# Optimization experiments

Measured on AMD Instinct MI355X. Metric: run time of the kernel, lower is better.

The kernel has to match this reference:

```python
import jax, jax.numpy as jnp
import numpy as np

EPS = 1e-5

def _bn(x, g, b, axes):
    m = jnp.mean(x, axes, keepdims=True)
    v = jnp.var(x, axes, keepdims=True)
    return (x - m) * jax.lax.rsqrt(v + EPS) * g + b

def _fps(p, m):
    # farthest point sampling: p [B,N,3] -> int32 indices [B,m]
    B, N, _ = p.shape
    def step(carry, _):
        mind, last = carry
        lastp = jnp.take_along_axis(p, last[:, None, None], axis=1)[:, 0]  # [B,3]
        d = jnp.sum((p - lastp[:, None, :]) ** 2, axis=-1)                 # [B,N]
        mind = jnp.minimum(mind, d)
        nxt = jnp.argmax(mind, axis=1).astype(jnp.int32)
        return (mind, nxt), last
    init = (jnp.full((B, N), jnp.inf, p.dtype), jnp.zeros((B,), jnp.int32))
    _, idxs = jax.lax.scan(step, init, None, length=m)  # [m,B]
    return idxs.T

def _gather(x, idx):
    # x [B,N,C], idx [B,...] -> [B,...,C]
    B, C = x.shape[0], x.shape[-1]
    flat = idx.reshape(B, -1)
    out = jnp.take_along_axis(x, flat[:, :, None], axis=1)
    return out.reshape(idx.shape + (C,))

def _transition_down(p, h, W, g, b, stride, nsample):
    # p [B,N,3], h [B,N,C] -> new_p [B,N//stride,3], y [B,N//stride,Cout]
    B, N, _ = p.shape
    M = N // stride
    idx = _fps(p, M)
    new_p = _gather(p, idx)                                               # [B,M,3]
    d = jnp.sum((new_p[:, :, None, :] - p[:, None, :, :]) ** 2, axis=-1)  # [B,M,N]
    _, nidx = jax.lax.top_k(-d, nsample)                                  # [B,M,k]
    gp = _gather(p, nidx) - new_p[:, :, None, :]                          # rel xyz [B,M,k,3]
    gx = _gather(h, nidx)                                                 # [B,M,k,C]
    feat = jnp.concatenate([gp, gx], axis=-1)                             # with_xyz=True
    y = jnp.einsum('bmkc,cd->bmkd', feat, W)
    y = jax.nn.relu(_bn(y, g, b, (0, 1, 2)))
    return new_p, jnp.max(y, axis=2)                                      # MaxPool1d(nsample)

def _forward(x, W1, g1, b1, W2, g2, b2, W3, g3, b3, W4, g4, b4, W5, g5, b5,
             Wc1, bc1, gc1, hc1, Wc2, bc2, gc2, hc2, Wc3, bc3):
    p = x[..., :3]                                    # in_channels == 3 -> features = xyz
    h = jnp.einsum('bnc,cd->bnd', p, W1)
    h = jax.nn.relu(_bn(h, g1, b1, (0, 1)))           # enc1: stride=1
    p, h = _transition_down(p, h, W2, g2, b2, 4, 16)  # enc2
    p, h = _transition_down(p, h, W3, g3, b3, 4, 16)  # enc3
    p, h = _transition_down(p, h, W4, g4, b4, 4, 16)  # enc4
    p, h = _transition_down(p, h, W5, g5, b5, 4, 16)  # enc5
    z = jnp.mean(h, axis=1)                           # segment-mean pool -> [B,512]
    z = jax.nn.relu(_bn(z @ Wc1 + bc1, gc1, hc1, (0,)))   # Dropout = identity (eval)
    z = jax.nn.relu(_bn(z @ Wc2 + bc2, gc2, hc2, (0,)))
    return z @ Wc3 + bc3                              # [B,40]

def setup_inputs() -> dict:
    key = jax.random.key(0)
    ks = jax.random.split(key, 16)
    B, N = 16, 4096
    def lin(k, fi, fo):
        return (jax.random.normal(k, (fi, fo), jnp.float32) / np.sqrt(fi)).astype(jnp.float32)
    inp = {"x": jax.random.normal(ks[0], (B, N, 3), jnp.float32)}
    planes = [32, 64, 128, 256, 512]
    ins = [3, 3 + 32, 3 + 64, 3 + 128, 3 + 256]
    for i, (fi, fo) in enumerate(zip(ins, planes), start=1):
        inp[f"W{i}"] = lin(ks[i], fi, fo)
        inp[f"g{i}"] = jnp.ones((fo,), jnp.float32)
        inp[f"b{i}"] = jnp.zeros((fo,), jnp.float32)
    dims = [(512, 256), (256, 128), (128, 40)]
    for j, (fi, fo) in enumerate(dims, start=1):
        inp[f"Wc{j}"] = lin(ks[5 + j], fi, fo)
        inp[f"bc{j}"] = jnp.zeros((fo,), jnp.float32)
        if j < 3:
            inp[f"gc{j}"] = jnp.ones((fo,), jnp.float32)
            inp[f"hc{j}"] = jnp.zeros((fo,), jnp.float32)
    return inp

def reference(x, W1, g1, b1, W2, g2, b2, W3, g3, b3, W4, g4, b4, W5, g5, b5,
              Wc1, bc1, gc1, hc1, Wc2, bc2, gc2, hc2, Wc3, bc3):
    return _forward(x, W1, g1, b1, W2, g2, b2, W3, g3, b3, W4, g4, b4, W5, g5, b5,
                    Wc1, bc1, gc1, hc1, Wc2, bc2, gc2, hc2, Wc3, bc3)
```

## Files before the change

### kernel.cpp

```cpp
#include <hip/hip_runtime.h>
#include <math.h>
#include <float.h>

#define BN_EPS 1e-5f

__device__ __forceinline__ float sqdist_exact(float dx, float dy, float dz) {
  return __fadd_rn(__fadd_rn(__fmul_rn(dx, dx), __fmul_rn(dy, dy)), __fmul_rn(dz, dz));
}

#define DPP_STEP(CTRL)                                                                   \
  {                                                                                      \
    unsigned int nhi = (unsigned int)__builtin_amdgcn_update_dpp((int)khi, (int)khi,     \
                                                                 CTRL, 0xf, 0xf, false); \
    unsigned int nlo = (unsigned int)__builtin_amdgcn_update_dpp((int)klo, (int)klo,     \
                                                                 CTRL, 0xf, 0xf, false); \
    unsigned long long nk = (((unsigned long long)nhi) << 32) | nlo;                     \
    if (nk > wk) { wk = nk; khi = nhi; klo = nlo; }                                      \
  }

template <int P, int NW>
__device__ __forceinline__ void fps_body(const float* __restrict__ pb,
                                         float* __restrict__ newp_b,
                                         float* spts, float* snew,
                                         unsigned long long* slots, int t) {
  constexpr int BS = NW * 64;
  constexpr int N = P * BS;
  constexpr int M = N / 4;
  const int wv = t >> 6;
  const int lane = t & 63;
  float px[P], py[P], pz[P], md[P];
#pragma unroll
  for (int j = 0; j < P; j++) {
    int i = j * BS + t;
    float x = pb[3 * i], y = pb[3 * i + 1], z = pb[3 * i + 2];
    px[j] = x; py[j] = y; pz[j] = z; md[j] = INFINITY;
    spts[3 * i] = x; spts[3 * i + 1] = y; spts[3 * i + 2] = z;
  }
  float lx = pb[0], ly = pb[1], lz = pb[2];
  if (t == 0) {
    if constexpr (NW > 1) {
      snew[0] = lx; snew[1] = ly; snew[2] = lz;
    } else {
      newp_b[0] = lx; newp_b[1] = ly; newp_b[2] = lz;
    }
  }

  for (int r = 1; r < M; r++) {
    float bv; int bi;
    {
      float d0 = sqdist_exact(px[0] - lx, py[0] - ly, pz[0] - lz);
      float m0 = fminf(md[0], d0);
      md[0] = m0;
      bv = m0; bi = t;
    }
#pragma unroll
    for (int j = 1; j < P; j++) {
      float d = sqdist_exact(px[j] - lx, py[j] - ly, pz[j] - lz);
      float m = fminf(md[j], d);
      md[j] = m;
      if (m > bv) { bv = m; bi = j * BS + t; }
    }
    unsigned int khi = __float_as_uint(bv);
    unsigned int klo = ~(unsigned int)bi;
    unsigned long long wk = (((unsigned long long)khi) << 32) | klo;
    DPP_STEP(0x111);
    DPP_STEP(0x112);
    DPP_STEP(0x114);
    DPP_STEP(0x118);
    DPP_STEP(0x142);
    DPP_STEP(0x143);
    unsigned int gidx;
    if constexpr (NW == 1) {
      unsigned int wlo = (unsigned int)__builtin_amdgcn_readlane((int)wk, 63);
      gidx = ~wlo;
    } else {
      unsigned long long* base = slots + (r & 1) * NW;
      if (lane == 63) base[wv] = wk;
      __syncthreads();
      unsigned long long fk = base[0];
#pragma unroll
      for (int w = 1; w < NW; w++) {
        unsigned long long k2 = base[w];
        if (k2 > fk) fk = k2;
      }
      gidx = ~(unsigned int)fk;
    }
    lx = spts[3 * gidx];
    ly = spts[3 * gidx + 1];
    lz = spts[3 * gidx + 2];
    if (t == 0) {
      if constexpr (NW > 1) {
        snew[3 * r] = lx; snew[3 * r + 1] = ly; snew[3 * r + 2] = lz;
      } else {
        newp_b[3 * r] = lx; newp_b[3 * r + 1] = ly; newp_b[3 * r + 2] = lz;
      }
    }
  }
  if constexpr (NW > 1) {
    __syncthreads();
    for (int i = t; i < M * 3; i += BS) newp_b[i] = snew[i];
  }
}

__device__ __forceinline__ void knn_body(const float* __restrict__ p,
                                         const float* __restrict__ newp,
                                         int N, int M, int BM,
                                         int* __restrict__ nidx,
                                         int gwid, int lane) {
  if (gwid >= BM) return;
  int b = gwid / M;
  const float* pb = p + (size_t)b * N * 3;
  float qx = newp[(size_t)gwid * 3], qy = newp[(size_t)gwid * 3 + 1], qz = newp[(size_t)gwid * 3 + 2];
  float bd[16];
  int bi[16];
#pragma unroll
  for (int s = 0; s < 16; s++) { bd[s] = INFINITY; bi[s] = 0x7FFFFFFF; }
  for (int c = lane; c < N; c += 64) {
    float d = sqdist_exact(pb[3 * c] - qx, pb[3 * c + 1] - qy, pb[3 * c + 2] - qz);
    if (d < bd[15]) {
      bd[15] = d; bi[15] = c;
#pragma unroll
      for (int s = 15; s >= 1; --s) {
        bool sw = bd[s] < bd[s - 1];
        if (sw) {
          float tf = bd[s]; bd[s] = bd[s - 1]; bd[s - 1] = tf;
          int ti = bi[s]; bi[s] = bi[s - 1]; bi[s - 1] = ti;
        }
      }
    }
  }
  int out = 0;
  for (int r = 0; r < 16; r++) {
    float v = bd[0]; int ii = bi[0];
    float mv = v; int mi = ii;
#pragma unroll
    for (int m = 1; m < 64; m <<= 1) {
      float v2 = __shfl_xor(mv, m);
      int i2 = __shfl_xor(mi, m);
      if (v2 < mv || (v2 == mv && i2 < mi)) { mv = v2; mi = i2; }
    }
    if (mi == ii) {
#pragma unroll
      for (int s = 0; s < 15; s++) { bd[s] = bd[s + 1]; bi[s] = bi[s + 1]; }
      bd[15] = INFINITY; bi[15] = 0x7FFFFFFF;
    }
    if (lane == r) out = mi;
  }
  if (lane < 16) nidx[(size_t)gwid * 16 + lane] = out;
}

__device__ __forceinline__ void stats_body(const float* __restrict__ v, int n, int D,
                                           float* __restrict__ partial, float* sm,
                                           int bid, int nb, int t) {
  int tid = bid * 256 + t;
  int stride = 256 * nb;
  float s = 0.f, q = 0.f;
  for (int i = tid; i < n; i += stride) { float a = v[i]; s += a; q += a * a; }
  int c = tid % D;
  for (int i = t; i < 2 * D; i += 256) sm[i] = 0.f;
  __syncthreads();
  atomicAdd(&sm[c], s);
  atomicAdd(&sm[D + c], q);
  __syncthreads();
  for (int i = t; i < 2 * D; i += 256)
    atomicAdd(&partial[(bid & 63) * 2 * D + i], sm[i]);
}

__device__ __forceinline__ void gemm_body(
    float* sm, const float* __restrict__ p, const float* __restrict__ h,
    const float* __restrict__ newp, const int* __restrict__ nidx,
    const float* __restrict__ W, float* __restrict__ ymax, float* __restrict__ ymin,
    float* __restrict__ partial, int N, int M, int BM, int Ch, int Cpad, int D,
    int Gseq, int bid, int t) {
  int Ctot = Ch + 3;
  int TD = D < 256 ? D : 256;
  int Gpar = 256 / TD;
  float* sfeat = sm;
  float* sstat = sm + Gpar * 16 * Cpad;
  for (int i = t; i < 2 * D; i += 256) sstat[i] = 0.f;
  int mloc = t / TD;
  int dbase = t % TD;
  int DV = D / TD;
  __syncthreads();
  for (int s = 0; s < Gseq; s++) {
    int grp0 = (bid * Gseq + s) * Gpar;
    if (grp0 >= BM) break;
    int nf = Gpar * 16 * Cpad;
    for (int i = t; i < nf; i += 256) {
      int c = i % Cpad;
      int rk = i / Cpad;
      int k = rk & 15;
      int g = rk >> 4;
      int grp = grp0 + g;
      float val = 0.f;
      if (grp < BM && c < Ctot) {
        int b = grp / M;
        int nb = nidx[(size_t)grp * 16 + k];
        if (c < 3)
          val = p[((size_t)b * N + nb) * 3 + c] - newp[(size_t)grp * 3 + c];
        else
          val = h[((size_t)b * N + nb) * Ch + (c - 3)];
      }
      sfeat[i] = val;
    }
    __syncthreads();
    int grp = grp0 + mloc;
    bool act = grp < BM;
    const float* fr = sfeat + mloc * 16 * Cpad;
    for (int dv = 0; dv < DV; ++dv) {
      int d = dbase + (dv << 8);
      float acc[16];
#pragma unroll
      for (int k = 0; k < 16; k++) acc[k] = 0.f;
      for (int c = 0; c < Cpad; c += 4) {
        float w0 = (c < Ctot) ? W[(size_t)c * D + d] : 0.f;
        float w1 = (c + 1 < Ctot) ? W[(size_t)(c + 1) * D + d] : 0.f;
        float w2 = (c + 2 < Ctot) ? W[(size_t)(c + 2) * D + d] : 0.f;
        float w3 = (c + 3 < Ctot) ? W[(size_t)(c + 3) * D + d] : 0.f;
#pragma unroll
        for (int k = 0; k < 16; k++) {
          const float4 f = *reinterpret_cast<const float4*>(fr + k * Cpad + c);
          acc[k] += f.x * w0 + f.y * w1 + f.z * w2 + f.w * w3;
        }
      }
      if (act) {
        float ssum = 0.f, ssq = 0.f, amax = -INFINITY, amin = INFINITY;
#pragma unroll
        for (int k = 0; k < 16; k++) {
          float a = acc[k];
          ssum += a; ssq += a * a;
          amax = fmaxf(amax, a); amin = fminf(amin, a);
        }
        ymax[(size_t)grp * D + d] = amax;
        ymin[(size_t)grp * D + d] = amin;
        atomicAdd(&sstat[d], ssum);
        atomicAdd(&sstat[D + d], ssq);
      }
    }
    __syncthreads();
  }
  for (int i = t; i < 2 * D; i += 256)
    atomicAdd(&partial[(bid & 63) * 2 * D + i], sstat[i]);
}

__global__ void __launch_bounds__(256) fused_fps1_mlp1_kernel(
    const float* __restrict__ x, float* __restrict__ newp,
    const float* __restrict__ W1, float* __restrict__ h1, int rows) {
  __shared__ float spts[4096 * 3];
  __shared__ float snew[1024 * 3];
  __shared__ unsigned long long slots[8];
  const int t = threadIdx.x;
  if (blockIdx.x < 16) {
    fps_body<16, 4>(x + (size_t)blockIdx.x * 4096 * 3, newp + (size_t)blockIdx.x * 1024 * 3,
                    spts, snew, slots, t);
  } else {
    int tid = (blockIdx.x - 16) * 256 + t;
    int row = tid >> 5;
    int d = tid & 31;
    if (row < rows) {
      float x0 = x[row * 3 + 0], x1 = x[row * 3 + 1], x2 = x[row * 3 + 2];
      h1[row * 32 + d] = x0 * W1[d] + x1 * W1[32 + d] + x2 * W1[64 + d];
    }
  }
}

__global__ void __launch_bounds__(256) fused_fks_kernel(
    const float* __restrict__ fp, float* __restrict__ fnewp,
    const float* __restrict__ kp, const float* __restrict__ knewp,
    int kN, int kM, int kBM, int* __restrict__ knidx, int nKnn,
    const float* __restrict__ sv, int sn, int sD, float* __restrict__ spartial, int nStats) {
  __shared__ float spts[1024 * 3];
  __shared__ float snew[256 * 3];
  __shared__ unsigned long long slots[8];
  __shared__ float ssm[64];
  const int t = threadIdx.x;
  const int bid = blockIdx.x;
  if (bid < 16) {
    fps_body<4, 4>(fp + (size_t)bid * 1024 * 3, fnewp + (size_t)bid * 256 * 3,
                   spts, snew, slots, t);
  } else if (bid < 16 + nKnn) {
    int gwid = ((bid - 16) * 256 + t) >> 6;
    knn_body(kp, knewp, kN, kM, kBM, knidx, gwid, t & 63);
  } else {
    stats_body(sv, sn, sD, spartial, ssm, bid - 16 - nKnn, nStats, t);
  }
}

template <int P, int NW>
__global__ void __launch_bounds__(256) fused_gfk_kernel(
    const float* __restrict__ p, const float* __restrict__ h,
    const float* __restrict__ newp, const int* __restrict__ nidx,
    const float* __restrict__ W, float* __restrict__ ymax, float* __restrict__ ymin,
    float* __restrict__ partial, int N, int M, int BM, int Ch, int Cpad, int D,
    int Gseq, int nGemm,
    const float* __restrict__ fp, float* __restrict__ fnewp, int nFps,
    const float* __restrict__ kp, const float* __restrict__ knewp,
    int kN, int kM, int kBM, int* __restrict__ knidx) {
  constexpr int FBS = NW * 64;
  constexpr int FN = P * FBS;
  constexpr int FM = FN / 4;
  __shared__ float spts[FN * 3];
  __shared__ float snew[NW > 1 ? FM * 3 : 1];
  __shared__ unsigned long long slots[NW > 1 ? 2 * NW : 2];
  extern __shared__ float sm[];
  const int t = threadIdx.x;
  const int bid = blockIdx.x;
  if (bid < nGemm) {
    gemm_body(sm, p, h, newp, nidx, W, ymax, ymin, partial,
              N, M, BM, Ch, Cpad, D, Gseq, bid, t);
  } else if (bid < nGemm + nFps) {
    int fb = bid - nGemm;
    if (NW > 1 || t < 64) {
      fps_body<P, NW>(fp + (size_t)fb * FN * 3, fnewp + (size_t)fb * FM * 3,
                      spts, snew, slots, t);
    }
  } else {
    int gwid = ((bid - nGemm - nFps) * 256 + t) >> 6;
    knn_body(kp, knewp, kN, kM, kBM, knidx, gwid, t & 63);
  }
}

__global__ void __launch_bounds__(256) gemm_kernel(
    const float* __restrict__ p, const float* __restrict__ h, const float* __restrict__ newp,
    const int* __restrict__ nidx, const float* __restrict__ W,
    float* __restrict__ ymax, float* __restrict__ ymin, float* __restrict__ partial,
    int N, int M, int BM, int Ch, int Cpad, int D, int Gseq) {
  extern __shared__ float sm[];
  gemm_body(sm, p, h, newp, nidx, W, ymax, ymin, partial,
            N, M, BM, Ch, Cpad, D, Gseq, blockIdx.x, threadIdx.x);
}

__global__ void __launch_bounds__(256) bn_fused_kernel(
    const float* __restrict__ partial, const float* __restrict__ g,
    const float* __restrict__ b, float cnt, int D,
    float* __restrict__ vmax, const float* __restrict__ vmin, int n) {
  extern __shared__ float ss[];
  int t = threadIdx.x;
  for (int d = t; d < D; d += 256) {
    float s = 0.f, q = 0.f;
    for (int j = 0; j < 64; j++) { s += partial[j * 2 * D + d]; q += partial[j * 2 * D + D + d]; }
    float mean = s / cnt;
    float var = fmaxf(q / cnt - mean * mean, 0.f);
    float sc = g[d] * rsqrtf(var + BN_EPS);
    ss[d] = sc;
    ss[D + d] = b[d] - mean * sc;
  }
  __syncthreads();
  int tid = blockIdx.x * 256 + t;
  int stride = 256 * gridDim.x;
  for (int i = tid; i < n; i += stride) {
    int d = i % D;
    float sc = ss[d], sh = ss[D + d];
    float v = (sc >= 0.f) ? vmax[i] : vmin[i];
    vmax[i] = fmaxf(v * sc + sh, 0.f);
  }
}

__global__ void __launch_bounds__(512) classifier_kernel(
    const float* __restrict__ h4,
    const float* __restrict__ Wc1, const float* __restrict__ bc1,
    const float* __restrict__ gc1, const float* __restrict__ hc1,
    const float* __restrict__ Wc2, const float* __restrict__ bc2,
    const float* __restrict__ gc2, const float* __restrict__ hc2,
    const float* __restrict__ Wc3, const float* __restrict__ bc3,
    float* __restrict__ out) {
  __shared__ float z[16 * 512];
  __shared__ float z1[16 * 256];
  __shared__ float z2[16 * 128];
  __shared__ float sc[256], sh[256];
  int t = threadIdx.x;
  for (int i = t; i < 16 * 512; i += 512) {
    int b = i >> 9, c = i & 511;
    float s = 0.f;
    for (int k = 0; k < 16; k++) s += h4[((size_t)b * 16 + k) * 512 + c];
    z[i] = s * (1.f / 16.f);
  }
  __syncthreads();
  for (int i = t; i < 16 * 256; i += 512) {
    int b = i >> 8, d = i & 255;
    float a = bc1[d];
    for (int c = 0; c < 512; c++) a += z[(b << 9) + c] * Wc1[c * 256 + d];
    z1[i] = a;
  }
  __syncthreads();
  if (t < 256) {
    float s = 0.f, q = 0.f;
    for (int b = 0; b < 16; b++) { float a = z1[(b << 8) + t]; s += a; q += a * a; }
    float mean = s * (1.f / 16.f);
    float var = fmaxf(q * (1.f / 16.f) - mean * mean, 0.f);
    float scl = gc1[t] * rsqrtf(var + BN_EPS);
    sc[t] = scl; sh[t] = hc1[t] - mean * scl;
  }
  __syncthreads();
  for (int i = t; i < 16 * 256; i += 512) {
    int d = i & 255;
    z1[i] = fmaxf(z1[i] * sc[d] + sh[d], 0.f);
  }
  __syncthreads();
  for (int i = t; i < 16 * 128; i += 512) {
    int b = i >> 7, d = i & 127;
    float a = bc2[d];
    for (int c = 0; c < 256; c++) a += z1[(b << 8) + c] * Wc2[c * 128 + d];
    z2[i] = a;
  }
  __syncthreads();
  if (t < 128) {
    float s = 0.f, q = 0.f;
    for (int b = 0; b < 16; b++) { float a = z2[(b << 7) + t]; s += a; q += a * a; }
    float mean = s * (1.f / 16.f);
    float var = fmaxf(q * (1.f / 16.f) - mean * mean, 0.f);
    float scl = gc2[t] * rsqrtf(var + BN_EPS);
    sc[t] = scl; sh[t] = hc2[t] - mean * scl;
  }
  __syncthreads();
  for (int i = t; i < 16 * 128; i += 512) {
    int d = i & 127;
    z2[i] = fmaxf(z2[i] * sc[d] + sh[d], 0.f);
  }
  __syncthreads();
  for (int i = t; i < 640; i += 512) {
    int b = i / 40, d = i % 40;
    float a = bc3[d];
    for (int c = 0; c < 128; c++) a += z2[(b << 7) + c] * Wc3[c * 40 + d];
    out[i] = a;
  }
}

extern "C" void kernel_launch(void* const* d_in, const int* in_sizes, int n_in,
                              void* d_out, int out_size, void* d_ws, size_t ws_size,
                              hipStream_t stream) {
  (void)in_sizes; (void)n_in; (void)out_size; (void)ws_size;
  const float* x   = (const float*)d_in[0];
  const float* W1  = (const float*)d_in[1];
  const float* g1  = (const float*)d_in[2];
  const float* b1  = (const float*)d_in[3];
  const float* W2  = (const float*)d_in[4];
  const float* g2  = (const float*)d_in[5];
  const float* b2  = (const float*)d_in[6];
  const float* W3  = (const float*)d_in[7];
  const float* g3  = (const float*)d_in[8];
  const float* b3  = (const float*)d_in[9];
  const float* W4  = (const float*)d_in[10];
  const float* g4  = (const float*)d_in[11];
  const float* b4  = (const float*)d_in[12];
  const float* W5  = (const float*)d_in[13];
  const float* g5  = (const float*)d_in[14];
  const float* b5  = (const float*)d_in[15];
  const float* Wc1 = (const float*)d_in[16];
  const float* bc1 = (const float*)d_in[17];
  const float* gc1 = (const float*)d_in[18];
  const float* hc1 = (const float*)d_in[19];
  const float* Wc2 = (const float*)d_in[20];
  const float* bc2 = (const float*)d_in[21];
  const float* gc2 = (const float*)d_in[22];
  const float* hc2 = (const float*)d_in[23];
  const float* Wc3 = (const float*)d_in[24];
  const float* bc3 = (const float*)d_in[25];
  float* out = (float*)d_out;

  float* ws = (float*)d_ws;
  float* HA    = ws;
  float* HB    = HA + 2097152;
  float* YMIN  = HB + 1048576;
  float* NP1   = YMIN + 1048576;
  float* NP2   = NP1 + 49152;
  float* NP3   = NP2 + 12288;
  float* NP4   = NP3 + 3072;
  int*   NIDX1 = (int*)(NP4 + 768);
  int*   NIDX2 = NIDX1 + 262144;
  int*   NIDX3 = NIDX2 + 65536;
  int*   NIDX4 = NIDX3 + 16384;
  float* PART  = (float*)(NIDX4 + 4096);

  hipMemsetAsync(PART, 0, 5 * 65536 * sizeof(float), stream);

  fused_fps1_mlp1_kernel<<<16 + 8192, 256, 0, stream>>>(x, NP1, W1, HA, 65536);

  fused_fks_kernel<<<16 + 4096 + 256, 256, 0, stream>>>(
      NP1, NP2, x, NP1, 4096, 1024, 16384, NIDX1, 4096,
      HA, 65536 * 32, 32, PART, 256);
  bn_fused_kernel<<<512, 256, 2 * 32 * sizeof(float), stream>>>(
      PART, g1, b1, 65536.f, 32, HA, HA, 65536 * 32);

  fused_gfk_kernel<4, 1><<<512 + 16 + 1024, 256, (4 * 16 * 36 + 2 * 64) * sizeof(float), stream>>>(
      x, HA, NP1, NIDX1, W2, HB, YMIN, PART + 65536, 4096, 1024, 16384, 32, 36, 64, 8, 512,
      NP2, NP3, 16,
      NP1, NP2, 1024, 256, 4096, NIDX2);
  bn_fused_kernel<<<512, 256, 2 * 64 * sizeof(float), stream>>>(
      PART + 65536, g2, b2, (float)(16384 * 16), 64, HB, YMIN, 16384 * 64);

  fused_gfk_kernel<1, 1><<<512 + 16 + 256, 256, (2 * 16 * 68 + 2 * 128) * sizeof(float), stream>>>(
      NP1, HB, NP2, NIDX2, W3, HA, YMIN, PART + 2 * 65536, 1024, 256, 4096, 64, 68, 128, 4, 512,
      NP3, NP4, 16,
      NP2, NP3, 256, 64, 1024, NIDX3);
  bn_fused_kernel<<<512, 256, 2 * 128 * sizeof(float), stream>>>(
      PART + 2 * 65536, g3, b3, (float)(4096 * 16), 128, HA, YMIN, 4096 * 128);

  fused_gfk_kernel<1, 1><<<512 + 0 + 64, 256, (16 * 132 + 2 * 256) * sizeof(float), stream>>>(
      NP2, HA, NP3, NIDX3, W4, HB, YMIN, PART + 3 * 65536, 256, 64, 1024, 128, 132, 256, 2, 512,
      nullptr, nullptr, 0,
      NP3, NP4, 64, 16, 256, NIDX4);
  bn_fused_kernel<<<256, 256, 2 * 256 * sizeof(float), stream>>>(
      PART + 3 * 65536, g4, b4, (float)(1024 * 16), 256, HB, YMIN, 1024 * 256);

  gemm_kernel<<<256, 256, (16 * 260 + 2 * 512) * sizeof(float), stream>>>(
      NP3, HB, NP4, NIDX4, W5, HA, YMIN, PART + 4 * 65536, 64, 16, 256, 256, 260, 512, 1);
  bn_fused_kernel<<<64, 256, 2 * 512 * sizeof(float), stream>>>(
      PART + 4 * 65536, g5, b5, (float)(256 * 16), 512, HA, YMIN, 256 * 512);

  classifier_kernel<<<1, 512, 0, stream>>>(HA, Wc1, bc1, gc1, hc1, Wc2, bc2, gc2, hc2, Wc3, bc3, out);
}
```

Measured before the change: 1.338 ms.

## Fold BN+ReLU into next stage's gather instead of separate passes

Removes the five standalone batch-norm/ReLU kernels. Each consumer (gather-GEMM blocks and the classifier) now recomputes the per-channel scale and shift from the partial statistics and applies BN+ReLU on the fly when loading features, choosing the max or min buffer by the sign of the scale. This saves kernel launches and full read/write passes over the activation buffers. In exchange, every GEMM block redundantly reduces 64 partials per channel, and the YMIN buffers are split in two so producer and consumer do not overlap.

```diff
diff --git a/kernel.cpp b/kernel.cpp
--- a/kernel.cpp
+++ b/kernel.cpp
@@ -168,8 +168,11 @@
 
 __device__ __forceinline__ void gemm_body(
     float* sm, const float* __restrict__ p, const float* __restrict__ h,
-    const float* __restrict__ newp, const int* __restrict__ nidx,
-    const float* __restrict__ W, float* __restrict__ ymax, float* __restrict__ ymin,
+    const float* __restrict__ hmin, const float* __restrict__ newp,
+    const int* __restrict__ nidx, const float* __restrict__ W,
+    const float* __restrict__ bnp, const float* __restrict__ bng,
+    const float* __restrict__ bnb, float bncnt,
+    float* __restrict__ ymax, float* __restrict__ ymin,
     float* __restrict__ partial, int N, int M, int BM, int Ch, int Cpad, int D,
     int Gseq, int bid, int t) {
   int Ctot = Ch + 3;
@@ -177,7 +180,17 @@
   int Gpar = 256 / TD;
   float* sfeat = sm;
   float* sstat = sm + Gpar * 16 * Cpad;
+  float* sbn   = sstat + 2 * D;
   for (int i = t; i < 2 * D; i += 256) sstat[i] = 0.f;
+  for (int d = t; d < Ch; d += 256) {
+    float s = 0.f, q = 0.f;
+    for (int j = 0; j < 64; j++) { s += bnp[j * 2 * Ch + d]; q += bnp[j * 2 * Ch + Ch + d]; }
+    float mean = s / bncnt;
+    float var = fmaxf(q / bncnt - mean * mean, 0.f);
+    float sc = bng[d] * rsqrtf(var + BN_EPS);
+    sbn[d] = sc;
+    sbn[Ch + d] = bnb[d] - mean * sc;
+  }
   int mloc = t / TD;
   int dbase = t % TD;
   int DV = D / TD;
@@ -196,10 +209,14 @@
       if (grp < BM && c < Ctot) {
         int b = grp / M;
         int nb = nidx[(size_t)grp * 16 + k];
-        if (c < 3)
+        if (c < 3) {
           val = p[((size_t)b * N + nb) * 3 + c] - newp[(size_t)grp * 3 + c];
-        else
-          val = h[((size_t)b * N + nb) * Ch + (c - 3)];
+        } else {
+          int cc = c - 3;
+          float sc = sbn[cc], sh = sbn[Ch + cc];
+          const float* hs = (sc >= 0.f) ? h : hmin;
+          val = fmaxf(hs[((size_t)b * N + nb) * Ch + cc] * sc + sh, 0.f);
+        }
       }
       sfeat[i] = val;
     }
@@ -289,8 +306,11 @@
 template <int P, int NW>
 __global__ void __launch_bounds__(256) fused_gfk_kernel(
     const float* __restrict__ p, const float* __restrict__ h,
-    const float* __restrict__ newp, const int* __restrict__ nidx,
-    const float* __restrict__ W, float* __restrict__ ymax, float* __restrict__ ymin,
+    const float* __restrict__ hmin, const float* __restrict__ newp,
+    const int* __restrict__ nidx, const float* __restrict__ W,
+    const float* __restrict__ bnp, const float* __restrict__ bng,
+    const float* __restrict__ bnb, float bncnt,
+    float* __restrict__ ymax, float* __restrict__ ymin,
     float* __restrict__ partial, int N, int M, int BM, int Ch, int Cpad, int D,
     int Gseq, int nGemm,
     const float* __restrict__ fp, float* __restrict__ fnewp, int nFps,
@@ -306,8 +326,8 @@
   const int t = threadIdx.x;
   const int bid = blockIdx.x;
   if (bid < nGemm) {
-    gemm_body(sm, p, h, newp, nidx, W, ymax, ymin, partial,
-              N, M, BM, Ch, Cpad, D, Gseq, bid, t);
+    gemm_body(sm, p, h, hmin, newp, nidx, W, bnp, bng, bnb, bncnt,
+              ymax, ymin, partial, N, M, BM, Ch, Cpad, D, Gseq, bid, t);
   } else if (bid < nGemm + nFps) {
     int fb = bid - nGemm;
     if (NW > 1 || t < 64) {
@@ -321,43 +341,22 @@
 }
 
 __global__ void __launch_bounds__(256) gemm_kernel(
-    const float* __restrict__ p, const float* __restrict__ h, const float* __restrict__ newp,
+    const float* __restrict__ p, const float* __restrict__ h,
+    const float* __restrict__ hmin, const float* __restrict__ newp,
     const int* __restrict__ nidx, const float* __restrict__ W,
-    float* __restrict__ ymax, float* __restrict__ ymin, float* __restrict__ partial,
-    int N, int M, int BM, int Ch, int Cpad, int D, int Gseq) {
+    const float* __restrict__ bnp, const float* __restrict__ bng,
+    const float* __restrict__ bnb, float bncnt,
+    float* __restrict__ ymax, float* __restrict__ ymin,
+    float* __restrict__ partial, int N, int M, int BM, int Ch, int Cpad, int D, int Gseq) {
   extern __shared__ float sm[];
-  gemm_body(sm, p, h, newp, nidx, W, ymax, ymin, partial,
-            N, M, BM, Ch, Cpad, D, Gseq, blockIdx.x, threadIdx.x);
-}
-
-__global__ void __launch_bounds__(256) bn_fused_kernel(
-    const float* __restrict__ partial, const float* __restrict__ g,
-    const float* __restrict__ b, float cnt, int D,
-    float* __restrict__ vmax, const float* __restrict__ vmin, int n) {
-  extern __shared__ float ss[];
-  int t = threadIdx.x;
-  for (int d = t; d < D; d += 256) {
-    float s = 0.f, q = 0.f;
-    for (int j = 0; j < 64; j++) { s += partial[j * 2 * D + d]; q += partial[j * 2 * D + D + d]; }
-    float mean = s / cnt;
-    float var = fmaxf(q / cnt - mean * mean, 0.f);
-    float sc = g[d] * rsqrtf(var + BN_EPS);
-    ss[d] = sc;
-    ss[D + d] = b[d] - mean * sc;
-  }
-  __syncthreads();
-  int tid = blockIdx.x * 256 + t;
-  int stride = 256 * gridDim.x;
-  for (int i = tid; i < n; i += stride) {
-    int d = i % D;
-    float sc = ss[d], sh = ss[D + d];
-    float v = (sc >= 0.f) ? vmax[i] : vmin[i];
-    vmax[i] = fmaxf(v * sc + sh, 0.f);
-  }
+  gemm_body(sm, p, h, hmin, newp, nidx, W, bnp, bng, bnb, bncnt,
+            ymax, ymin, partial, N, M, BM, Ch, Cpad, D, Gseq, blockIdx.x, threadIdx.x);
 }
 
 __global__ void __launch_bounds__(512) classifier_kernel(
-    const float* __restrict__ h4,
+    const float* __restrict__ h4, const float* __restrict__ h4min,
+    const float* __restrict__ bnp, const float* __restrict__ bng,
+    const float* __restrict__ bnb, float bncnt,
     const float* __restrict__ Wc1, const float* __restrict__ bc1,
     const float* __restrict__ gc1, const float* __restrict__ hc1,
     const float* __restrict__ Wc2, const float* __restrict__ bc2,
@@ -368,11 +367,25 @@
   __shared__ float z1[16 * 256];
   __shared__ float z2[16 * 128];
   __shared__ float sc[256], sh[256];
+  __shared__ float s5[1024];
   int t = threadIdx.x;
+  for (int d = t; d < 512; d += 512) {
+    float s = 0.f, q = 0.f;
+    for (int j = 0; j < 64; j++) { s += bnp[j * 1024 + d]; q += bnp[j * 1024 + 512 + d]; }
+    float mean = s / bncnt;
+    float var = fmaxf(q / bncnt - mean * mean, 0.f);
+    float scv = bng[d] * rsqrtf(var + BN_EPS);
+    s5[d] = scv;
+    s5[512 + d] = bnb[d] - mean * scv;
+  }
+  __syncthreads();
   for (int i = t; i < 16 * 512; i += 512) {
     int b = i >> 9, c = i & 511;
+    float scv = s5[c], shv = s5[512 + c];
+    const float* src = (scv >= 0.f) ? h4 : h4min;
     float s = 0.f;
-    for (int k = 0; k < 16; k++) s += h4[((size_t)b * 16 + k) * 512 + c];
+    for (int k = 0; k < 16; k++)
+      s += fmaxf(src[((size_t)b * 16 + k) * 512 + c] * scv + shv, 0.f);
     z[i] = s * (1.f / 16.f);
   }
   __syncthreads();
@@ -461,8 +474,9 @@
   float* ws = (float*)d_ws;
   float* HA    = ws;
   float* HB    = HA + 2097152;
-  float* YMIN  = HB + 1048576;
-  float* NP1   = YMIN + 1048576;
+  float* YMINA = HB + 1048576;
+  float* YMINB = YMINA + 1048576;
+  float* NP1   = YMINB + 524288;
   float* NP2   = NP1 + 49152;
   float* NP3   = NP2 + 12288;
   float* NP4   = NP3 + 3072;
@@ -479,34 +493,33 @@
   fused_fks_kernel<<<16 + 4096 + 256, 256, 0, stream>>>(
       NP1, NP2, x, NP1, 4096, 1024, 16384, NIDX1, 4096,
       HA, 65536 * 32, 32, PART, 256);
-  bn_fused_kernel<<<512, 256, 2 * 32 * sizeof(float), stream>>>(
-      PART, g1, b1, 65536.f, 32, HA, HA, 65536 * 32);
-
-  fused_gfk_kernel<4, 1><<<512 + 16 + 1024, 256, (4 * 16 * 36 + 2 * 64) * sizeof(float), stream>>>(
-      x, HA, NP1, NIDX1, W2, HB, YMIN, PART + 65536, 4096, 1024, 16384, 32, 36, 64, 8, 512,
+
+  fused_gfk_kernel<4, 1><<<512 + 16 + 1024, 256,
+                           (4 * 16 * 36 + 2 * 64 + 2 * 32) * sizeof(float), stream>>>(
+      x, HA, HA, NP1, NIDX1, W2, PART, g1, b1, 65536.f,
+      HB, YMINA, PART + 65536, 4096, 1024, 16384, 32, 36, 64, 8, 512,
       NP2, NP3, 16,
       NP1, NP2, 1024, 256, 4096, NIDX2);
-  bn_fused_kernel<<<512, 256, 2 * 64 * sizeof(float), stream>>>(
-      PART + 65536, g2, b2, (float)(16384 * 16), 64, HB, YMIN, 16384 * 64);
-
-  fused_gfk_kernel<1, 1><<<512 + 16 + 256, 256, (2 * 16 * 68 + 2 * 128) * sizeof(float), stream>>>(
-      NP1, HB, NP2, NIDX2, W3, HA, YMIN, PART + 2 * 65536, 1024, 256, 4096, 64, 68, 128, 4, 512,
+
+  fused_gfk_kernel<1, 1><<<512 + 16 + 256, 256,
+                           (2 * 16 * 68 + 2 * 128 + 2 * 64) * sizeof(float), stream>>>(
+      NP1, HB, YMINA, NP2, NIDX2, W3, PART + 65536, g2, b2, (float)(16384 * 16),
+      HA, YMINB, PART + 2 * 65536, 1024, 256, 4096, 64, 68, 128, 4, 512,
       NP3, NP4, 16,
       NP2, NP3, 256, 64, 1024, NIDX3);
-  bn_fused_kernel<<<512, 256, 2 * 128 * sizeof(float), stream>>>(
-      PART + 2 * 65536, g3, b3, (float)(4096 * 16), 128, HA, YMIN, 4096 * 128);
-
-  fused_gfk_kernel<1, 1><<<512 + 0 + 64, 256, (16 * 132 + 2 * 256) * sizeof(float), stream>>>(
-      NP2, HA, NP3, NIDX3, W4, HB, YMIN, PART + 3 * 65536, 256, 64, 1024, 128, 132, 256, 2, 512,
+
+  fused_gfk_kernel<1, 1><<<512 + 0 + 64, 256,
+                           (16 * 132 + 2 * 256 + 2 * 128) * sizeof(float), stream>>>(
+      NP2, HA, YMINB, NP3, NIDX3, W4, PART + 2 * 65536, g3, b3, (float)(4096 * 16),
+      HB, YMINA, PART + 3 * 65536, 256, 64, 1024, 128, 132, 256, 2, 512,
       nullptr, nullptr, 0,
       NP3, NP4, 64, 16, 256, NIDX4);
-  bn_fused_kernel<<<256, 256, 2 * 256 * sizeof(float), stream>>>(
-      PART + 3 * 65536, g4, b4, (float)(1024 * 16), 256, HB, YMIN, 1024 * 256);
-
-  gemm_kernel<<<256, 256, (16 * 260 + 2 * 512) * sizeof(float), stream>>>(
-      NP3, HB, NP4, NIDX4, W5, HA, YMIN, PART + 4 * 65536, 64, 16, 256, 256, 260, 512, 1);
-  bn_fused_kernel<<<64, 256, 2 * 512 * sizeof(float), stream>>>(
-      PART + 4 * 65536, g5, b5, (float)(256 * 16), 512, HA, YMIN, 256 * 512);
-
-  classifier_kernel<<<1, 512, 0, stream>>>(HA, Wc1, bc1, gc1, hc1, Wc2, bc2, gc2, hc2, Wc3, bc3, out);
-}
+
+  gemm_kernel<<<256, 256, (16 * 260 + 2 * 512 + 2 * 256) * sizeof(float), stream>>>(
+      NP3, HB, YMINA, NP4, NIDX4, W5, PART + 3 * 65536, g4, b4, (float)(1024 * 16),
+      HA, YMINB, PART + 4 * 65536, 64, 16, 256, 256, 260, 512, 1);
+
+  classifier_kernel<<<1, 512, 0, stream>>>(
+      HA, YMINB, PART + 4 * 65536, g5, b5, (float)(256 * 16),
+      Wc1, bc1, gc1, hc1, Wc2, bc2, gc2, hc2, Wc3, bc3, out);
+}
```

After: 1.329 ms, median of 2. Within noise of the previous version (-0.6%).
